# Kernel optimization log

Hardware: AMD Instinct MI355X
Metric: run time of the kernel (lower is better)

The kernel has to match this reference:

```python
import jax, jax.numpy as jnp
import numpy as np

N = 100000   # nodes
E = 1600000  # edges
IN = 32      # in_channels
H = 64       # hidden_channels
L = 16       # latent_dim
G = 64       # graphs in batch


def setup_inputs() -> dict:
    key = jax.random.key(0)
    ks = jax.random.split(key, 20)
    def w(k, shape, fan):
        return jax.random.normal(k, shape, jnp.float32) * (1.0 / np.sqrt(fan))
    inp = {}
    inp["x"] = jax.random.normal(ks[0], (N, IN), jnp.float32)
    inp["edge_index"] = jax.random.randint(ks[1], (2, E), 0, N)
    inp["batch"] = jnp.sort(jax.random.randint(ks[2], (N,), 0, G))
    # encoder GCN convs: in->h, h->h, h->h
    inp["W_enc0"] = w(ks[3], (IN, H), IN); inp["b_enc0"] = jnp.zeros((H,), jnp.float32)
    inp["W_enc1"] = w(ks[4], (H, H), H);   inp["b_enc1"] = jnp.zeros((H,), jnp.float32)
    inp["W_enc2"] = w(ks[5], (H, H), H);   inp["b_enc2"] = jnp.zeros((H,), jnp.float32)
    # latent projection and decoder projection
    inp["W_proj"] = w(ks[6], (H, L), H);   inp["b_proj"] = jnp.zeros((L,), jnp.float32)
    inp["W_dec_proj"] = w(ks[7], (L, H), L); inp["b_dec_proj"] = jnp.zeros((H,), jnp.float32)
    # decoder GCN convs: h->h, h->in
    inp["W_dec0"] = w(ks[8], (H, H), H);   inp["b_dec0"] = jnp.zeros((H,), jnp.float32)
    inp["W_dec1"] = w(ks[9], (H, IN), H);  inp["b_dec1"] = jnp.zeros((IN,), jnp.float32)
    return inp


def gcn_conv(x, W, b, src, dst, dinv):
    xw = x @ W                                   # [N, out]
    coef = (dinv[src] * dinv[dst])[:, None]      # [E, 1]
    out = jax.ops.segment_sum(xw[src] * coef, dst, num_segments=N)
    out = out + xw * (dinv * dinv)[:, None]      # self-loop contribution
    return out + b


def reference(x, edge_index, batch,
              W_enc0, b_enc0, W_enc1, b_enc1, W_enc2, b_enc2,
              W_proj, b_proj, W_dec_proj, b_dec_proj,
              W_dec0, b_dec0, W_dec1, b_dec1):
    src, dst = edge_index[0], edge_index[1]
    # degree with self-loops (computed on target nodes, PyG default)
    deg = jax.ops.segment_sum(jnp.ones((E,), jnp.float32), dst, num_segments=N) + 1.0
    dinv = jax.lax.rsqrt(deg)
    # encoder (eval mode: dropout is identity)
    h = jax.nn.relu(gcn_conv(x, W_enc0, b_enc0, src, dst, dinv))
    h = jax.nn.relu(gcn_conv(h, W_enc1, b_enc1, src, dst, dinv))
    h = jax.nn.relu(gcn_conv(h, W_enc2, b_enc2, src, dst, dinv))
    # global mean pool over graph ids
    sums = jax.ops.segment_sum(h, batch, num_segments=G)
    cnt = jax.ops.segment_sum(jnp.ones((N,), jnp.float32), batch, num_segments=G)
    g = sums / jnp.maximum(cnt, 1.0)[:, None]    # [G, H]
    z = g @ W_proj + b_proj                      # [G, L]
    # decoder: broadcast z back to nodes, project, two GCN convs
    d = jax.nn.relu(z[batch] @ W_dec_proj + b_dec_proj)
    d = jax.nn.relu(gcn_conv(d, W_dec0, b_dec0, src, dst, dinv))
    x_recon = gcn_conv(d, W_dec1, b_dec1, src, dst, dinv)
    return (x_recon, z)
```

## Files before the change

kernel.cpp:

```cpp
#include <hip/hip_runtime.h>
#include <hip/hip_bf16.h>

typedef unsigned long long u64;

static constexpr int IN_CH  = 32;
static constexpr int HID    = 64;
static constexpr int LAT    = 16;
static constexpr int NGRAPH = 64;
static constexpr int CPB     = 4;


__device__ inline void add4(float4& a, const float4& b) {
    a.x += b.x; a.y += b.y; a.z += b.z; a.w += b.w;
}


__global__ __launch_bounds__(256) void bhist_kernel(const int* __restrict__ ei,
                                                    int* __restrict__ bh, int E) {
    __shared__ int lh[256];
    lh[threadIdx.x] = 0;
    __syncthreads();
    int base = blockIdx.x * 2048;
    #pragma unroll
    for (int j = 0; j < 8; j++) {
        int idx = base + j * 256 + threadIdx.x;
        if (idx < E) atomicAdd(&lh[ei[E + idx] >> 9], 1);
    }
    __syncthreads();
    if (lh[threadIdx.x]) atomicAdd(&bh[threadIdx.x], lh[threadIdx.x]);
}


__global__ __launch_bounds__(256) void bin_kernel(
        const int* __restrict__ ei, const int* __restrict__ bh,
        int* __restrict__ gcur, u64* __restrict__ sout, int E) {
    __shared__ int lhist[256], lscan[256], lcur[256], gbase[256], bbaseL[256];
    __shared__ u64 sbuf[2048];
    int tid = threadIdx.x;
    lhist[tid] = 0;
    {
        int v = bh[tid];
        lscan[tid] = v;
        for (int off = 1; off < 256; off <<= 1) {
            __syncthreads();
            int x = (tid >= off) ? lscan[tid - off] : 0;
            __syncthreads();
            lscan[tid] += x;
        }
        __syncthreads();
        bbaseL[tid] = lscan[tid] - v;
    }
    __syncthreads();
    int base = blockIdx.x * 2048;
    int cnt = min(2048, E - base);
    int myb[8]; u64 myp[8];
    #pragma unroll
    for (int j = 0; j < 8; j++) {
        int idx = base + j * 256 + tid;
        myb[j] = -1;
        if (idx < E) {
            int key = ei[E + idx], val = ei[idx];
            int b = key >> 9;
            myb[j] = b;
            myp[j] = ((u64)(unsigned)key << 32) | (unsigned)val;
            atomicAdd(&lhist[b], 1);
        }
    }
    __syncthreads();
    int v = lhist[tid];
    lscan[tid] = v;
    for (int off = 1; off < 256; off <<= 1) {
        __syncthreads();
        int x = (tid >= off) ? lscan[tid - off] : 0;
        __syncthreads();
        lscan[tid] += x;
    }
    __syncthreads();
    int excl = lscan[tid] - v;
    __syncthreads();
    lscan[tid] = excl;
    lcur[tid] = excl;
    __syncthreads();
    #pragma unroll
    for (int j = 0; j < 8; j++) {
        if (myb[j] >= 0) {
            int pos = atomicAdd(&lcur[myb[j]], 1);
            sbuf[pos] = myp[j];
        }
    }
    gbase[tid] = v ? atomicAdd(&gcur[tid], v) : 0;
    __syncthreads();
    for (int i = tid; i < cnt; i += 256) {
        u64 p = sbuf[i];
        int b = (int)(p >> 41);
        sout[bbaseL[b] + gbase[b] + (i - lscan[b])] = p;
    }
}


__global__ __launch_bounds__(256) void degb_kernel(
        const u64* __restrict__ staged, const int* __restrict__ bh,
        const int* __restrict__ batch,
        int* __restrict__ rank, int* __restrict__ perm, int* __restrict__ cnt2,
        int* __restrict__ rowptr2, float* __restrict__ dinvR,
        float2* __restrict__ pgR, int* __restrict__ bbase, int N, int E) {
    __shared__ int sc[256];
    __shared__ int ldeg[512], lrank[512], degS[512], psum[512];
    __shared__ int kcur[256];
    __shared__ int s0s, s1s;
    int b = blockIdx.x, tid = threadIdx.x;
    {
        int bv = bh[tid];
        sc[tid] = bv;
        for (int off = 1; off < 256; off <<= 1) {
            __syncthreads();
            int x = (tid >= off) ? sc[tid - off] : 0;
            __syncthreads();
            sc[tid] += x;
        }
        __syncthreads();
        if (tid == b) { s0s = sc[tid] - bv; s1s = sc[tid]; }
    }
    ldeg[tid] = 0; ldeg[tid + 256] = 0;
    degS[tid] = 0; degS[tid + 256] = 0;
    kcur[tid] = 0;
    __syncthreads();
    int s0 = s0s, s1 = s1s;
    int base = b << 9;
    for (int i = s0 + tid; i < s1; i += 256)
        atomicAdd(&ldeg[(int)(__builtin_nontemporal_load(&staged[i]) >> 32) - base], 1);
    __syncthreads();
    int k = N - base; k = k < 0 ? 0 : (k > 512 ? 512 : k);
    #pragma unroll
    for (int j = 0; j < 2; j++) {
        int t = tid + j * 256;
        if (t < k) atomicAdd(&kcur[min(ldeg[t], 255)], 1);
    }
    __syncthreads();
    {
        int hv = kcur[tid];
        sc[tid] = hv;
        for (int off = 1; off < 256; off <<= 1) {
            __syncthreads();
            int x = (tid >= off) ? sc[tid - off] : 0;
            __syncthreads();
            sc[tid] += x;
        }
        __syncthreads();
        kcur[tid] = sc[tid] - hv;
    }
    __syncthreads();
    #pragma unroll
    for (int j = 0; j < 2; j++) {
        int t = tid + j * 256;
        if (t < k) lrank[t] = atomicAdd(&kcur[min(ldeg[t], 255)], 1);
    }
    __syncthreads();
    #pragma unroll
    for (int j = 0; j < 2; j++) {
        int t = tid + j * 256;
        if (t < k) degS[lrank[t]] = ldeg[t];
    }
    __syncthreads();
    {
        int v0 = degS[2 * tid], v1 = degS[2 * tid + 1];
        int T = v0 + v1;
        sc[tid] = T;
        for (int off = 1; off < 256; off <<= 1) {
            __syncthreads();
            int x = (tid >= off) ? sc[tid - off] : 0;
            __syncthreads();
            sc[tid] += x;
        }
        __syncthreads();
        int ex = sc[tid] - T;
        psum[2 * tid] = ex;
        psum[2 * tid + 1] = ex + v0;
    }
    __syncthreads();
    #pragma unroll
    for (int j = 0; j < 2; j++) {
        int t = tid + j * 256;
        if (t < k) {
            int n = base + t;
            int d = ldeg[t], lr = lrank[t];
            int r = base + lr;
            rank[n] = r;
            perm[r] = n;
            cnt2[r] = d;
            rowptr2[r] = s0 + psum[lr];
            float dv = rsqrtf((float)d + 1.0f);
            dinvR[r] = dv;
            pgR[r] = make_float2(dv, __int_as_float(batch[n]));
        }
    }
    if (tid == 0) {
        bbase[b] = s0;
        if (b == 255) bbase[256] = E;
    }
}


__global__ __launch_bounds__(256) void csr_kernel(
        const u64* __restrict__ staged, const int* __restrict__ bbase,
        const int* __restrict__ rank, const int* __restrict__ rowptr2,
        int* __restrict__ col) {
    __shared__ int lcur[512];
    int b = blockIdx.x, tid = threadIdx.x;
    lcur[tid] = 0; lcur[tid + 256] = 0;
    __syncthreads();
    int s0 = bbase[b], s1 = bbase[b + 1];
    int base = b << 9;
    for (int i = s0 + tid; i < s1; i += 256) {
        u64 p = __builtin_nontemporal_load(&staged[i]);
        int dst = (int)(p >> 32);
        int src = (int)(p & 0xffffffffu);
        int rd = rank[dst];
        int pos = rowptr2[rd] + atomicAdd(&lcur[rd - base], 1);
        col[pos] = rank[src];
    }
}


__global__ void slice_x_kernel(const float* __restrict__ x, const int* __restrict__ perm,
                               const float* __restrict__ dinvR,
                               float* __restrict__ xs, int N) {
    int idx = blockIdx.x * 256 + threadIdx.x;
    if (idx >= N * 2) return;
    int r = idx >> 1, h = idx & 1;
    int sl = blockIdx.y;
    int n = perm[r];
    float4 v = ((const float4*)x)[(size_t)n * 8 + sl * 2 + h];
    float dn = dinvR[r];
    v.x *= dn; v.y *= dn; v.z *= dn; v.w *= dn;
    ((float4*)(xs + (size_t)sl * N * 8))[idx] = v;
}


template <int C, bool ADD_BIAS, bool OUT_ROWMAJOR>
__global__ __launch_bounds__(256) void agg_kernel(
        const float* __restrict__ in, float* __restrict__ out,
        const int* __restrict__ rowptr2, const int* __restrict__ cnt2,
        const int* __restrict__ col, const float* __restrict__ dinvR,
        const int* __restrict__ perm, const float* __restrict__ bias,
        int nbk, int N) {
    constexpr int NSL = C / 8;
    int sl = blockIdx.x % NSL;
    int o  = blockIdx.x / NSL;
    int chunk = (o % nbk) * CPB + (o / nbk);
    int slot = threadIdx.x >> 1, h = threadIdx.x & 1;
    int r = chunk * 128 + slot;
    if (r >= N) return;
    const float4* inS = (const float4*)(in + (size_t)sl * N * 8);
    int start = rowptr2[r], m = cnt2[r];
    const int* cp = col + start;
    float4 acc0 = inS[(size_t)r * 2 + h];
    float4 acc1 = make_float4(0.f, 0.f, 0.f, 0.f);
    int i = 0;
    for (; i + 16 <= m; i += 16) {
        int4 ca = *(const int4*)(cp + i);
        int4 cb = *(const int4*)(cp + i + 4);
        int4 cc = *(const int4*)(cp + i + 8);
        int4 cd = *(const int4*)(cp + i + 12);
        float4 v0 = inS[(size_t)ca.x*2+h], v1 = inS[(size_t)ca.y*2+h];
        float4 v2 = inS[(size_t)ca.z*2+h], v3 = inS[(size_t)ca.w*2+h];
        float4 v4 = inS[(size_t)cb.x*2+h], v5 = inS[(size_t)cb.y*2+h];
        float4 v6 = inS[(size_t)cb.z*2+h], v7 = inS[(size_t)cb.w*2+h];
        float4 v8 = inS[(size_t)cc.x*2+h], v9 = inS[(size_t)cc.y*2+h];
        float4 va = inS[(size_t)cc.z*2+h], vb = inS[(size_t)cc.w*2+h];
        float4 vc = inS[(size_t)cd.x*2+h], vd = inS[(size_t)cd.y*2+h];
        float4 ve = inS[(size_t)cd.z*2+h], vf = inS[(size_t)cd.w*2+h];
        add4(v0, v1); add4(v2, v3); add4(v4, v5); add4(v6, v7);
        add4(v8, v9); add4(va, vb); add4(vc, vd); add4(ve, vf);
        add4(v0, v2); add4(v4, v6); add4(v8, va); add4(vc, ve);
        add4(v0, v4); add4(v8, vc);
        add4(acc0, v0); add4(acc1, v8);
    }
    if (i + 8 <= m) {
        int4 ca = *(const int4*)(cp + i);
        int4 cb = *(const int4*)(cp + i + 4);
        float4 v0 = inS[(size_t)ca.x*2+h], v1 = inS[(size_t)ca.y*2+h];
        float4 v2 = inS[(size_t)ca.z*2+h], v3 = inS[(size_t)ca.w*2+h];
        float4 v4 = inS[(size_t)cb.x*2+h], v5 = inS[(size_t)cb.y*2+h];
        float4 v6 = inS[(size_t)cb.z*2+h], v7 = inS[(size_t)cb.w*2+h];
        add4(v0, v1); add4(v2, v3); add4(v4, v5); add4(v6, v7);
        add4(v0, v2); add4(v4, v6);
        add4(acc0, v0); add4(acc1, v4);
        i += 8;
    }
    if (i + 4 <= m) {
        int4 ca = *(const int4*)(cp + i);
        float4 v0 = inS[(size_t)ca.x*2+h], v1 = inS[(size_t)ca.y*2+h];
        float4 v2 = inS[(size_t)ca.z*2+h], v3 = inS[(size_t)ca.w*2+h];
        add4(v0, v1); add4(v2, v3); add4(v0, v2);
        add4(acc0, v0);
        i += 4;
    }
    for (; i < m; ++i) {
        int c = cp[i];
        add4(acc1, inS[(size_t)c * 2 + h]);
    }
    add4(acc0, acc1);
    float dn = dinvR[r];
    acc0.x *= dn; acc0.y *= dn; acc0.z *= dn; acc0.w *= dn;
    if (ADD_BIAS) {
        float4 b4 = ((const float4*)bias)[sl * 2 + h];
        add4(acc0, b4);
    }
    if (OUT_ROWMAJOR) ((float4*)out)[(size_t)perm[r] * (C / 4) + sl * 2 + h] = acc0;
    else ((float4*)(out + (size_t)sl * N * 8))[(size_t)r * 2 + h] = acc0;
}


__global__ __launch_bounds__(256) void gagg_kernel(
        const float* __restrict__ dg, const float2* __restrict__ pgR,
        const int* __restrict__ rowptr2, const int* __restrict__ cnt2,
        const int* __restrict__ col, float* __restrict__ out, int nbk, int N) {
    __shared__ float dgL[NGRAPH * 68];
    for (int i = threadIdx.x; i < NGRAPH * 64; i += 256)
        dgL[(i >> 6) * 68 + (i & 63)] = dg[i];
    __syncthreads();
    int slot = threadIdx.x >> 1, e = threadIdx.x & 1;
    int o = blockIdx.x;
    int chunk = (o % nbk) * CPB + (o / nbk);
    int r = chunk * 128 + slot;
    if (r >= N) return;
    const float4* dgL4 = (const float4*)dgL;
    int start = rowptr2[r], m = cnt2[r];
    const int* cp = col + start;
    float2 ps = pgR[r];
    float dn = ps.x;
    int gs = __float_as_int(ps.y);
    float4 acc[8];
    {
        const float4* rp = dgL4 + gs * 17 + e * 8;
        #pragma unroll
        for (int j = 0; j < 8; ++j) {
            float4 v = rp[j];
            acc[j] = make_float4(dn * v.x, dn * v.y, dn * v.z, dn * v.w);
        }
    }
    int i = 0;
    for (; i + 4 <= m; i += 4) {
        int4 ca = *(const int4*)(cp + i);
        float2 p0 = pgR[ca.x], p1 = pgR[ca.y], p2 = pgR[ca.z], p3 = pgR[ca.w];
        const float4* r0 = dgL4 + __float_as_int(p0.y) * 17 + e * 8;
        const float4* r1 = dgL4 + __float_as_int(p1.y) * 17 + e * 8;
        const float4* r2 = dgL4 + __float_as_int(p2.y) * 17 + e * 8;
        const float4* r3 = dgL4 + __float_as_int(p3.y) * 17 + e * 8;
        float w0 = p0.x, w1 = p1.x, w2 = p2.x, w3 = p3.x;
        #pragma unroll
        for (int j = 0; j < 8; ++j) {
            float4 v0 = r0[j], v1 = r1[j], v2 = r2[j], v3 = r3[j];
            acc[j].x += (w0 * v0.x + w1 * v1.x) + (w2 * v2.x + w3 * v3.x);
            acc[j].y += (w0 * v0.y + w1 * v1.y) + (w2 * v2.y + w3 * v3.y);
            acc[j].z += (w0 * v0.z + w1 * v1.z) + (w2 * v2.z + w3 * v3.z);
            acc[j].w += (w0 * v0.w + w1 * v1.w) + (w2 * v2.w + w3 * v3.w);
        }
    }
    for (; i < m; ++i) {
        int c0 = cp[i];
        float2 p0 = pgR[c0];
        const float4* r0 = dgL4 + __float_as_int(p0.y) * 17 + e * 8;
        float w0 = p0.x;
        #pragma unroll
        for (int j = 0; j < 8; ++j) {
            float4 v0 = r0[j];
            acc[j].x += w0 * v0.x; acc[j].y += w0 * v0.y;
            acc[j].z += w0 * v0.z; acc[j].w += w0 * v0.w;
        }
    }
    #pragma unroll
    for (int k = 0; k < 4; ++k) {
        #pragma unroll
        for (int jj = 0; jj < 2; ++jj) {
            float4 v = acc[k * 2 + jj];
            v.x *= dn; v.y *= dn; v.z *= dn; v.w *= dn;
            ((float4*)(out + (size_t)(4 * e + k) * N * 8))[(size_t)r * 2 + jj] = v;
        }
    }
}


template <int CIN, int COUT, bool RELU, bool BIAS, bool SCALE, bool OUT_ROWMAJOR>
__global__ __launch_bounds__(256) void gemm_kernel(
        const float* __restrict__ in, const float* __restrict__ W,
        const float* __restrict__ b, const float* __restrict__ dinvR,
        const int* __restrict__ perm, float* __restrict__ out, int N) {
    constexpr int NPB = 256 / COUT;
    constexpr int K4 = CIN / 4;
    __shared__ float4 xsh[NPB * K4];
    int r  = threadIdx.x / COUT;
    int co = threadIdx.x % COUT;
    float w[CIN];
    #pragma unroll
    for (int k = 0; k < CIN; ++k) w[k] = W[k * COUT + co];
    float bsv = BIAS ? b[co] : 0.f;
    int ngroups = (N + NPB - 1) / NPB;
    for (int grp = blockIdx.x; grp < ngroups; grp += gridDim.x) {
        int base = grp * NPB;
        __syncthreads();
        for (int i = threadIdx.x; i < NPB * K4; i += 256) {
            int rr = i / K4, k4 = i % K4;
            int n = base + rr;
            float4 v = make_float4(0.f, 0.f, 0.f, 0.f);
            if (n < N) v = ((const float4*)(in + (size_t)(k4 >> 1) * N * 8))[(size_t)n * 2 + (k4 & 1)];
            xsh[i] = v;
        }
        __syncthreads();
        int n = base + r;
        if (n < N) {
            float acc = bsv;
            #pragma unroll
            for (int k4 = 0; k4 < K4; ++k4) {
                float4 xv = xsh[r * K4 + k4];
                acc += xv.x * w[4 * k4] + xv.y * w[4 * k4 + 1]
                     + xv.z * w[4 * k4 + 2] + xv.w * w[4 * k4 + 3];
            }
            if (RELU) acc = fmaxf(acc, 0.f);
            if (SCALE) acc *= dinvR[n];
            if (OUT_ROWMAJOR) out[(size_t)perm[n] * COUT + co] = acc;
            else out[(size_t)(co >> 3) * N * 8 + (size_t)n * 8 + (co & 7)] = acc;
        }
    }
}


__global__ __launch_bounds__(256) void gemm2_kernel(
        const float* __restrict__ in, const float* __restrict__ W0,
        const float* __restrict__ b0, const float* __restrict__ W1,
        const float* __restrict__ dinvR, float* __restrict__ out, int N) {
    constexpr int NPB = 4;
    __shared__ float4 xsh[NPB * 16];
    __shared__ float t1sh[NPB * 65];
    __shared__ float w1sh[HID * IN_CH];
    int tid = threadIdx.x;
    int r  = tid >> 6;
    int co = tid & 63;
    float w0[HID];
    #pragma unroll
    for (int k = 0; k < HID; ++k) w0[k] = W0[k * HID + co];
    float b0v = b0[co];
    for (int i = tid; i < HID * IN_CH; i += 256) w1sh[i] = W1[i];
    int r2  = tid >> 5;
    int co2 = tid & 31;
    int ngroups = (N + NPB - 1) / NPB;
    for (int grp = blockIdx.x; grp < ngroups; grp += gridDim.x) {
        int base = grp * NPB;
        __syncthreads();
        if (tid < NPB * 16) {
            int rr = tid >> 4, k4 = tid & 15;
            int n = base + rr;
            float4 v = make_float4(0.f, 0.f, 0.f, 0.f);
            if (n < N) v = ((const float4*)(in + (size_t)(k4 >> 1) * N * 8))[(size_t)n * 2 + (k4 & 1)];
            xsh[tid] = v;
        }
        __syncthreads();
        {
            float acc = b0v;
            #pragma unroll
            for (int k4 = 0; k4 < 16; ++k4) {
                float4 xv = xsh[r * 16 + k4];
                acc += xv.x * w0[4 * k4] + xv.y * w0[4 * k4 + 1]
                     + xv.z * w0[4 * k4 + 2] + xv.w * w0[4 * k4 + 3];
            }
            t1sh[r * 65 + co] = fmaxf(acc, 0.f);
        }
        __syncthreads();
        if (r2 < NPB) {
            int n = base + r2;
            if (n < N) {
                float acc = 0.f;
                #pragma unroll
                for (int k = 0; k < HID; ++k)
                    acc += t1sh[r2 * 65 + k] * w1sh[k * IN_CH + co2];
                acc *= dinvR[n];
                out[(size_t)(co2 >> 3) * N * 8 + (size_t)n * 8 + (co2 & 7)] = acc;
            }
        }
    }
}


__global__ __launch_bounds__(256) void pool_kernel(
        const float* __restrict__ h, const int* __restrict__ batch,
        float* __restrict__ sums, int* __restrict__ cntb, int N) {
    const int CHUNK = 512;
    int chunkStart = blockIdx.x * CHUNK;
    int c = threadIdx.x & 63;
    int r = threadIdx.x >> 6;
    int curg = -1;
    float acc = 0.f;
    int cnt = 0;
    int end = chunkStart + CHUNK;
    if (end > N) end = N;
    for (int n = chunkStart + r; n < end; n += 4) {
        int g = batch[n];
        if (g != curg) {
            if (curg >= 0) {
                atomicAdd(&sums[curg * 64 + c], acc);
                if (c == 0) atomicAdd(&cntb[curg], cnt);
            }
            curg = g; acc = 0.f; cnt = 0;
        }
        acc += h[(size_t)n * 64 + c];
        cnt++;
    }
    if (curg >= 0) {
        atomicAdd(&sums[curg * 64 + c], acc);
        if (c == 0) atomicAdd(&cntb[curg], cnt);
    }
}


__global__ __launch_bounds__(1024) void latent_kernel(
        const float* __restrict__ sums, const int* __restrict__ cntb,
        const float* __restrict__ Wp, const float* __restrict__ bp,
        const float* __restrict__ Wd, const float* __restrict__ bd,
        float* __restrict__ z_out, float* __restrict__ dg) {
    __shared__ float zl[NGRAPH * LAT];
    int t = threadIdx.x;
    {
        int g = t / LAT, l = t % LAT;
        float cf = (float)cntb[g];
        float inv = 1.0f / fmaxf(cf, 1.0f);
        float acc = bp[l];
        #pragma unroll
        for (int k = 0; k < HID; k++) acc += sums[g * HID + k] * inv * Wp[k * LAT + l];
        zl[t] = acc;
        z_out[t] = acc;
    }
    __syncthreads();
    #pragma unroll
    for (int i = 0; i < 4; i++) {
        int idx = t + i * 1024;
        int g = idx >> 6, c = idx & 63;
        float acc = bd[c];
        #pragma unroll
        for (int l = 0; l < LAT; l++) acc += zl[g * LAT + l] * Wd[l * HID + c];
        dg[idx] = fmaxf(acc, 0.f);
    }
}


extern "C" void kernel_launch(void* const* d_in, const int* in_sizes, int n_in,
                              void* d_out, int out_size, void* d_ws, size_t ws_size,
                              hipStream_t stream) {
    const float* x          = (const float*)d_in[0];
    const int*   ei         = (const int*)d_in[1];
    const int*   batch      = (const int*)d_in[2];
    const float* W_enc0     = (const float*)d_in[3];
    const float* b_enc0     = (const float*)d_in[4];
    const float* W_enc1     = (const float*)d_in[5];
    const float* b_enc1     = (const float*)d_in[6];
    const float* W_enc2     = (const float*)d_in[7];
    const float* b_enc2     = (const float*)d_in[8];
    const float* W_proj     = (const float*)d_in[9];
    const float* b_proj     = (const float*)d_in[10];
    const float* W_dec_proj = (const float*)d_in[11];
    const float* b_dec_proj = (const float*)d_in[12];
    const float* W_dec0     = (const float*)d_in[13];
    const float* b_dec0     = (const float*)d_in[14];
    const float* W_dec1     = (const float*)d_in[15];
    const float* b_dec1     = (const float*)d_in[16];

    const int N = in_sizes[0] / IN_CH;
    const int E = in_sizes[1] / 2;

    char* ws = (char*)d_ws;
    size_t off = 0;
    auto alloc = [&](size_t bytes) {
        void* p = ws + off;
        off += (bytes + 255) & ~(size_t)255;
        return p;
    };
    float* A       = (float*)alloc((size_t)N * HID * 4);
    float* B       = (float*)alloc((size_t)N * HID * 4);
    float* XS      = (float*)alloc((size_t)N * IN_CH * 4);
    int*   col     = (int*)  alloc((size_t)E * 4);
    int*   cnt2    = (int*)  alloc((size_t)N * 4);
    int*   rowptr2 = (int*)  alloc((size_t)(N + 1) * 4);
    int*   perm    = (int*)  alloc((size_t)N * 4);
    int*   rank    = (int*)  alloc((size_t)N * 4);
    float* dinvR   = (float*)alloc((size_t)N * 4);
    float2* pgR    = (float2*)alloc((size_t)N * 8);
    int*   bbase   = (int*)  alloc(257 * 4);
    char* zbase = ws + off;
    int*   bh      = (int*)  alloc(256 * 4);
    int*   gcurD   = (int*)  alloc(256 * 4);
    float* sums    = (float*)alloc((size_t)NGRAPH * HID * 4);
    int*   cntb    = (int*)  alloc((size_t)NGRAPH * 4);
    size_t zbytes = (size_t)((ws + off) - zbase);
    float* dg      = (float*)alloc((size_t)NGRAPH * HID * 4);

    u64* staged1 = (u64*)XS;

    float* x_recon = (float*)d_out;
    float* z_out   = (float*)d_out + (size_t)N * IN_CH;

    hipMemsetAsync(zbase, 0, zbytes, stream);

    int ebins = (E + 2047) / 2048;
    int nbk = (N + 511) >> 9;
    int chunksI = nbk * CPB;

    bhist_kernel<<<ebins, 256, 0, stream>>>(ei, bh, E);
    bin_kernel<<<ebins, 256, 0, stream>>>(ei, bh, gcurD, staged1, E);
    degb_kernel<<<256, 256, 0, stream>>>(staged1, bh, batch, rank, perm, cnt2,
                                         rowptr2, dinvR, pgR, bbase, N, E);
    csr_kernel<<<256, 256, 0, stream>>>(staged1, bbase, rank, rowptr2, col);

    {
        dim3 g((N * 2 + 255) / 256, IN_CH / 8);
        slice_x_kernel<<<g, 256, 0, stream>>>(x, perm, dinvR, XS, N);
    }

    agg_kernel<IN_CH, false, false><<<chunksI * 4, 256, 0, stream>>>(
        XS, A, rowptr2, cnt2, col, dinvR, perm, nullptr, nbk, N);
    gemm_kernel<IN_CH, HID, true, true, true, false><<<2048, 256, 0, stream>>>(
        A, W_enc0, b_enc0, dinvR, perm, B, N);
    agg_kernel<HID, false, false><<<chunksI * 8, 256, 0, stream>>>(
        B, A, rowptr2, cnt2, col, dinvR, perm, nullptr, nbk, N);
    gemm_kernel<HID, HID, true, true, true, false><<<2048, 256, 0, stream>>>(
        A, W_enc1, b_enc1, dinvR, perm, B, N);
    agg_kernel<HID, false, false><<<chunksI * 8, 256, 0, stream>>>(
        B, A, rowptr2, cnt2, col, dinvR, perm, nullptr, nbk, N);
    gemm_kernel<HID, HID, true, true, false, true><<<2048, 256, 0, stream>>>(
        A, W_enc2, b_enc2, dinvR, perm, B, N);

    pool_kernel<<<(N + 511) / 512, 256, 0, stream>>>(B, batch, sums, cntb, N);
    latent_kernel<<<1, 1024, 0, stream>>>(sums, cntb, W_proj, b_proj, W_dec_proj, b_dec_proj, z_out, dg);

    gagg_kernel<<<chunksI, 256, 0, stream>>>(dg, pgR, rowptr2, cnt2, col, A, nbk, N);
    gemm2_kernel<<<2048, 256, 0, stream>>>(A, W_dec0, b_dec0, W_dec1, dinvR, B, N);
    agg_kernel<IN_CH, true, true><<<chunksI * 4, 256, 0, stream>>>(
        B, x_recon, rowptr2, cnt2, col, dinvR, perm, b_dec1, nbk, N);
}
```

Measured before the change: 635.8 us.

## Widen channel slices from 8 to 16 floats for gather aggregation

Changes the sliced feature layout from 8-channel to 16-channel slices, so each node's slice row is 64 bytes and is read by four threads per row instead of two. The aggregation kernel processes 64 rows per block with 8 chunks per bucket, drops the 16-wide unroll, and cuts the number of slice passes (and thus repeated col-index reads) in half. The producer kernels (slice_x, gemm, gemm2, gagg) are updated to write and read the new layout. Fewer passes over the CSR indices mean less index traffic, at the cost of less unrolling per thread and a larger random-gather footprint per slice.

```diff
diff --git a/kernel.cpp b/kernel.cpp
--- a/kernel.cpp
+++ b/kernel.cpp
@@ -7,7 +7,8 @@
 static constexpr int HID    = 64;
 static constexpr int LAT    = 16;
 static constexpr int NGRAPH = 64;
-static constexpr int CPB     = 4;
+static constexpr int CPB8   = 8;
+static constexpr int CPB4   = 4;
 
 
 __device__ inline void add4(float4& a, const float4& b) {
@@ -226,14 +227,14 @@
                                const float* __restrict__ dinvR,
                                float* __restrict__ xs, int N) {
     int idx = blockIdx.x * 256 + threadIdx.x;
-    if (idx >= N * 2) return;
-    int r = idx >> 1, h = idx & 1;
+    if (idx >= N * 4) return;
+    int r = idx >> 2, h = idx & 3;
     int sl = blockIdx.y;
     int n = perm[r];
-    float4 v = ((const float4*)x)[(size_t)n * 8 + sl * 2 + h];
+    float4 v = ((const float4*)x)[(size_t)n * 8 + sl * 4 + h];
     float dn = dinvR[r];
     v.x *= dn; v.y *= dn; v.z *= dn; v.w *= dn;
-    ((float4*)(xs + (size_t)sl * N * 8))[idx] = v;
+    ((float4*)(xs + (size_t)sl * N * 16))[idx] = v;
 }
 
 
@@ -244,71 +245,51 @@
         const int* __restrict__ col, const float* __restrict__ dinvR,
         const int* __restrict__ perm, const float* __restrict__ bias,
         int nbk, int N) {
-    constexpr int NSL = C / 8;
+    constexpr int NSL = C / 16;
     int sl = blockIdx.x % NSL;
     int o  = blockIdx.x / NSL;
-    int chunk = (o % nbk) * CPB + (o / nbk);
-    int slot = threadIdx.x >> 1, h = threadIdx.x & 1;
-    int r = chunk * 128 + slot;
+    int chunk = (o % nbk) * CPB8 + (o / nbk);
+    int quad = threadIdx.x >> 2, q = threadIdx.x & 3;
+    int r = chunk * 64 + quad;
     if (r >= N) return;
-    const float4* inS = (const float4*)(in + (size_t)sl * N * 8);
+    const float4* inS = (const float4*)(in + (size_t)sl * N * 16);
     int start = rowptr2[r], m = cnt2[r];
     const int* cp = col + start;
-    float4 acc0 = inS[(size_t)r * 2 + h];
+    float4 acc0 = inS[(size_t)r * 4 + q];
     float4 acc1 = make_float4(0.f, 0.f, 0.f, 0.f);
     int i = 0;
-    for (; i + 16 <= m; i += 16) {
+    for (; i + 8 <= m; i += 8) {
         int4 ca = *(const int4*)(cp + i);
         int4 cb = *(const int4*)(cp + i + 4);
-        int4 cc = *(const int4*)(cp + i + 8);
-        int4 cd = *(const int4*)(cp + i + 12);
-        float4 v0 = inS[(size_t)ca.x*2+h], v1 = inS[(size_t)ca.y*2+h];
-        float4 v2 = inS[(size_t)ca.z*2+h], v3 = inS[(size_t)ca.w*2+h];
-        float4 v4 = inS[(size_t)cb.x*2+h], v5 = inS[(size_t)cb.y*2+h];
-        float4 v6 = inS[(size_t)cb.z*2+h], v7 = inS[(size_t)cb.w*2+h];
-        float4 v8 = inS[(size_t)cc.x*2+h], v9 = inS[(size_t)cc.y*2+h];
-        float4 va = inS[(size_t)cc.z*2+h], vb = inS[(size_t)cc.w*2+h];
-        float4 vc = inS[(size_t)cd.x*2+h], vd = inS[(size_t)cd.y*2+h];
-        float4 ve = inS[(size_t)cd.z*2+h], vf = inS[(size_t)cd.w*2+h];
-        add4(v0, v1); add4(v2, v3); add4(v4, v5); add4(v6, v7);
-        add4(v8, v9); add4(va, vb); add4(vc, vd); add4(ve, vf);
-        add4(v0, v2); add4(v4, v6); add4(v8, va); add4(vc, ve);
-        add4(v0, v4); add4(v8, vc);
-        add4(acc0, v0); add4(acc1, v8);
-    }
-    if (i + 8 <= m) {
-        int4 ca = *(const int4*)(cp + i);
-        int4 cb = *(const int4*)(cp + i + 4);
-        float4 v0 = inS[(size_t)ca.x*2+h], v1 = inS[(size_t)ca.y*2+h];
-        float4 v2 = inS[(size_t)ca.z*2+h], v3 = inS[(size_t)ca.w*2+h];
-        float4 v4 = inS[(size_t)cb.x*2+h], v5 = inS[(size_t)cb.y*2+h];
-        float4 v6 = inS[(size_t)cb.z*2+h], v7 = inS[(size_t)cb.w*2+h];
+        float4 v0 = inS[(size_t)ca.x*4+q], v1 = inS[(size_t)ca.y*4+q];
+        float4 v2 = inS[(size_t)ca.z*4+q], v3 = inS[(size_t)ca.w*4+q];
+        float4 v4 = inS[(size_t)cb.x*4+q], v5 = inS[(size_t)cb.y*4+q];
+        float4 v6 = inS[(size_t)cb.z*4+q], v7 = inS[(size_t)cb.w*4+q];
         add4(v0, v1); add4(v2, v3); add4(v4, v5); add4(v6, v7);
         add4(v0, v2); add4(v4, v6);
         add4(acc0, v0); add4(acc1, v4);
-        i += 8;
     }
     if (i + 4 <= m) {
         int4 ca = *(const int4*)(cp + i);
-        float4 v0 = inS[(size_t)ca.x*2+h], v1 = inS[(size_t)ca.y*2+h];
-        float4 v2 = inS[(size_t)ca.z*2+h], v3 = inS[(size_t)ca.w*2+h];
+        float4 v0 = inS[(size_t)ca.x*4+q], v1 = inS[(size_t)ca.y*4+q];
+        float4 v2 = inS[(size_t)ca.z*4+q], v3 = inS[(size_t)ca.w*4+q];
         add4(v0, v1); add4(v2, v3); add4(v0, v2);
         add4(acc0, v0);
         i += 4;
     }
     for (; i < m; ++i) {
         int c = cp[i];
-        add4(acc1, inS[(size_t)c * 2 + h]);
+        add4(acc1, inS[(size_t)c * 4 + q]);
     }
     add4(acc0, acc1);
     float dn = dinvR[r];
     acc0.x *= dn; acc0.y *= dn; acc0.z *= dn; acc0.w *= dn;
     if (ADD_BIAS) {
-        float4 b4 = ((const float4*)bias)[sl * 2 + h];
+        float4 b4 = ((const float4*)bias)[sl * 4 + q];
         add4(acc0, b4);
     }
-    if (OUT_ROWMAJOR) ((float4*)out)[(size_t)perm[r] * (C / 4) + sl * 2 + h] = acc0;
-    else ((float4*)(out + (size_t)sl * N * 8))[(size_t)r * 2 + h] = acc0;
+    if (OUT_ROWMAJOR) ((float4*)out)[(size_t)perm[r] * (C / 4) + sl * 4 + q] = acc0;
+    else ((float4*)(out + (size_t)sl * N * 16))[(size_t)r * 4 + q] = acc0;
 }
 
 
@@ -322,7 +303,7 @@
     __syncthreads();
     int slot = threadIdx.x >> 1, e = threadIdx.x & 1;
     int o = blockIdx.x;
-    int chunk = (o % nbk) * CPB + (o / nbk);
+    int chunk = (o % nbk) * CPB4 + (o / nbk);
     int r = chunk * 128 + slot;
     if (r >= N) return;
     const float4* dgL4 = (const float4*)dgL;
@@ -376,7 +357,8 @@
         for (int jj = 0; jj < 2; ++jj) {
             float4 v = acc[k * 2 + jj];
             v.x *= dn; v.y *= dn; v.z *= dn; v.w *= dn;
-            ((float4*)(out + (size_t)(4 * e + k) * N * 8))[(size_t)r * 2 + jj] = v;
+            int ch = e * 32 + k * 8 + jj * 4;
+            ((float4*)(out + (size_t)(ch >> 4) * N * 16))[(size_t)r * 4 + ((ch & 15) >> 2)] = v;
         }
     }
 }
@@ -404,7 +386,7 @@
             int rr = i / K4, k4 = i % K4;
             int n = base + rr;
             float4 v = make_float4(0.f, 0.f, 0.f, 0.f);
-            if (n < N) v = ((const float4*)(in + (size_t)(k4 >> 1) * N * 8))[(size_t)n * 2 + (k4 & 1)];
+            if (n < N) v = ((const float4*)(in + (size_t)(k4 >> 2) * N * 16))[(size_t)n * 4 + (k4 & 3)];
             xsh[i] = v;
         }
         __syncthreads();
@@ -420,7 +402,7 @@
             if (RELU) acc = fmaxf(acc, 0.f);
             if (SCALE) acc *= dinvR[n];
             if (OUT_ROWMAJOR) out[(size_t)perm[n] * COUT + co] = acc;
-            else out[(size_t)(co >> 3) * N * 8 + (size_t)n * 8 + (co & 7)] = acc;
+            else out[(size_t)(co >> 4) * N * 16 + (size_t)n * 16 + (co & 15)] = acc;
         }
     }
 }
@@ -452,7 +434,7 @@
             int rr = tid >> 4, k4 = tid & 15;
             int n = base + rr;
             float4 v = make_float4(0.f, 0.f, 0.f, 0.f);
-            if (n < N) v = ((const float4*)(in + (size_t)(k4 >> 1) * N * 8))[(size_t)n * 2 + (k4 & 1)];
+            if (n < N) v = ((const float4*)(in + (size_t)(k4 >> 2) * N * 16))[(size_t)n * 4 + (k4 & 3)];
             xsh[tid] = v;
         }
         __syncthreads();
@@ -475,7 +457,7 @@
                 for (int k = 0; k < HID; ++k)
                     acc += t1sh[r2 * 65 + k] * w1sh[k * IN_CH + co2];
                 acc *= dinvR[n];
-                out[(size_t)(co2 >> 3) * N * 8 + (size_t)n * 8 + (co2 & 7)] = acc;
+                out[(size_t)(co2 >> 4) * N * 16 + (size_t)n * 16 + (co2 & 15)] = acc;
             }
         }
     }
@@ -602,7 +584,8 @@
 
     int ebins = (E + 2047) / 2048;
     int nbk = (N + 511) >> 9;
-    int chunksI = nbk * CPB;
+    int chunks8 = nbk * CPB8;
+    int chunks4 = nbk * CPB4;
 
     bhist_kernel<<<ebins, 256, 0, stream>>>(ei, bh, E);
     bin_kernel<<<ebins, 256, 0, stream>>>(ei, bh, gcurD, staged1, E);
@@ -611,19 +594,19 @@
     csr_kernel<<<256, 256, 0, stream>>>(staged1, bbase, rank, rowptr2, col);
 
     {
-        dim3 g((N * 2 + 255) / 256, IN_CH / 8);
+        dim3 g((N * 4 + 255) / 256, IN_CH / 16);
         slice_x_kernel<<<g, 256, 0, stream>>>(x, perm, dinvR, XS, N);
     }
 
-    agg_kernel<IN_CH, false, false><<<chunksI * 4, 256, 0, stream>>>(
+    agg_kernel<IN_CH, false, false><<<chunks8 * 2, 256, 0, stream>>>(
         XS, A, rowptr2, cnt2, col, dinvR, perm, nullptr, nbk, N);
     gemm_kernel<IN_CH, HID, true, true, true, false><<<2048, 256, 0, stream>>>(
         A, W_enc0, b_enc0, dinvR, perm, B, N);
-    agg_kernel<HID, false, false><<<chunksI * 8, 256, 0, stream>>>(
+    agg_kernel<HID, false, false><<<chunks8 * 4, 256, 0, stream>>>(
         B, A, rowptr2, cnt2, col, dinvR, perm, nullptr, nbk, N);
     gemm_kernel<HID, HID, true, true, true, false><<<2048, 256, 0, stream>>>(
         A, W_enc1, b_enc1, dinvR, perm, B, N);
-    agg_kernel<HID, false, false><<<chunksI * 8, 256, 0, stream>>>(
+    agg_kernel<HID, false, false><<<chunks8 * 4, 256, 0, stream>>>(
         B, A, rowptr2, cnt2, col, dinvR, perm, nullptr, nbk, N);
     gemm_kernel<HID, HID, true, true, false, true><<<2048, 256, 0, stream>>>(
         A, W_enc2, b_enc2, dinvR, perm, B, N);
@@ -631,8 +614,8 @@
     pool_kernel<<<(N + 511) / 512, 256, 0, stream>>>(B, batch, sums, cntb, N);
     latent_kernel<<<1, 1024, 0, stream>>>(sums, cntb, W_proj, b_proj, W_dec_proj, b_dec_proj, z_out, dg);
 
-    gagg_kernel<<<chunksI, 256, 0, stream>>>(dg, pgR, rowptr2, cnt2, col, A, nbk, N);
+    gagg_kernel<<<chunks4, 256, 0, stream>>>(dg, pgR, rowptr2, cnt2, col, A, nbk, N);
     gemm2_kernel<<<2048, 256, 0, stream>>>(A, W_dec0, b_dec0, W_dec1, dinvR, B, N);
-    agg_kernel<IN_CH, true, true><<<chunksI * 4, 256, 0, stream>>>(
+    agg_kernel<IN_CH, true, true><<<chunks8 * 2, 256, 0, stream>>>(
         B, x_recon, rowptr2, cnt2, col, dinvR, perm, b_dec1, nbk, N);
 }
```

Result: faster. 603.3 us (-5.1%).
